# Kernel optimization log

Hardware: AMD Instinct MI355X
Metric: run time of the kernel (lower is better)

## Reference

```python
import jax, jax.numpy as jnp
import numpy as np
import math

MUL = 32
E = 131072
N = 10000
IRREPS = [(0, 1), (1, -1), (2, 1)]  # (l, parity) for 0e + 1o + 2e
SQRT3 = math.sqrt(3.0)

_f = math.factorial


def _w3j_symbol(j1, j2, j3, m1, m2, m3):
    """Standard (complex-basis) Wigner 3j symbol via the Racah formula."""
    if m1 + m2 + m3 != 0:
        return 0.0
    if abs(m1) > j1 or abs(m2) > j2 or abs(m3) > j3:
        return 0.0
    if not (abs(j1 - j2) <= j3 <= j1 + j2):
        return 0.0
    tri = _f(j1 + j2 - j3) * _f(j1 - j2 + j3) * _f(-j1 + j2 + j3) / _f(j1 + j2 + j3 + 1)
    pref = (-1) ** (j1 - j2 - m3) * math.sqrt(
        tri * _f(j1 + m1) * _f(j1 - m1) * _f(j2 + m2) * _f(j2 - m2) * _f(j3 + m3) * _f(j3 - m3)
    )
    tmin = max(0, j2 - j3 - m1, j1 - j3 + m2)
    tmax = min(j1 + j2 - j3, j1 - m1, j2 + m2)
    s = 0.0
    for t in range(tmin, tmax + 1):
        s += (-1) ** t / (
            _f(t) * _f(j3 - j2 + t + m1) * _f(j3 - j1 + t - m2)
            * _f(j1 + j2 - j3 - t) * _f(j1 - t - m1) * _f(j2 - t + m2)
        )
    return pref * s


def _real_basis(l):
    """Complex -> real spherical-harmonic change of basis, rows m=-l..l."""
    U = np.zeros((2 * l + 1, 2 * l + 1), dtype=np.complex128)
    U[l, l] = 1.0
    s = 1.0 / math.sqrt(2.0)
    for m in range(1, l + 1):
        U[l + m, l + m] = ((-1) ** m) * s
        U[l + m, l - m] = s
        U[l - m, l - m] = 1j * s
        U[l - m, l + m] = -1j * ((-1) ** m) * s
    return U


def _w3j_real(l1, l2, l3):
    """Real-basis Wigner 3j tensor, Frobenius norm 1 (e3nn normalization)."""
    Wc = np.zeros((2 * l1 + 1, 2 * l2 + 1, 2 * l3 + 1), dtype=np.complex128)
    for m1 in range(-l1, l1 + 1):
        for m2 in range(-l2, l2 + 1):
            for m3 in range(-l3, l3 + 1):
                Wc[l1 + m1, l2 + m2, l3 + m3] = _w3j_symbol(l1, l2, l3, m1, m2, m3)
    C = np.einsum('im,jn,ko,mno->ijk', _real_basis(l1), _real_basis(l2), _real_basis(l3), Wc)
    re, im = C.real, C.imag
    R = re if np.linalg.norm(re) >= np.linalg.norm(im) else im
    return R / np.linalg.norm(R)


def _build_w3j():
    dims = [2 * l + 1 for l, _ in IRREPS]
    offs = np.concatenate([[0], np.cumsum(dims)])[:-1]
    base_dim = int(sum(dims))  # 9
    # auto-generated instructions: same loop order as the torch module
    ins = []
    for io, (lo, po) in enumerate(IRREPS):
        for i1, (l1, p1) in enumerate(IRREPS):
            for i2, (l2, p2) in enumerate(IRREPS):
                if p1 * p2 == po and abs(l1 - l2) <= lo <= l1 + l2:
                    ins.append((i1, i2, io))
    P = len(ins)  # 11 paths
    w3j = np.zeros((P, base_dim, base_dim, base_dim), dtype=np.float32)
    for p, (i1, i2, io) in enumerate(ins):
        l1, l2, lo = IRREPS[i1][0], IRREPS[i2][0], IRREPS[io][0]
        C = _w3j_real(l1, l2, lo) * math.sqrt(2 * lo + 1)  # component normalization
        w3j[p, offs[i1]:offs[i1] + dims[i1], offs[i2]:offs[i2] + dims[i2], offs[io]:offs[io] + dims[io]] = C
    return w3j


def setup_inputs() -> dict:
    key = jax.random.key(0)
    k1, k2, k3, k4 = jax.random.split(key, 4)
    w3j = jnp.asarray(_build_w3j())  # [P=11, 9, 9, 9]
    P = w3j.shape[0]
    base_dim = w3j.shape[1]
    return {
        'x1': jax.random.normal(k1, (E, MUL * base_dim), dtype=jnp.float32),
        'x2': jax.random.normal(k2, (E, MUL * base_dim), dtype=jnp.float32),
        'idxs': jax.random.randint(k3, (E,), 0, N),
        'weights': jax.random.uniform(k4, (MUL, P), dtype=jnp.float32, minval=-SQRT3, maxval=SQRT3),
        'w3j': w3j,
        'scatter_dim_size': N,
    }


def reference(x1, x2, idxs, weights, w3j, scatter_dim_size):
    base1 = w3j.shape[1]
    base2 = w3j.shape[2]
    # scatter edges -> nodes, then gather back per edge (neighbor sum per center)
    x2s = jax.ops.segment_sum(x2, idxs, num_segments=int(scatter_dim_size))
    x2g = x2s[idxs]
    x1r = x1.reshape(-1, MUL, base1)   # [E, u, i]
    x2r = x2g.reshape(-1, MUL, base2)  # [E, u, j]
    # path-channel coupled weighting: 'up,pijk->uijk'
    ww3j = jnp.einsum('up,pijk->uijk', weights, w3j)
    # out[e,u,k] = sum_ij x1[e,u,i] x2[e,u,j] ww3j[u,i,j,k]
    out = jnp.einsum('eui,euj,uijk->euk', x1r, x2r, ww3j)
    return out
```

## Files before the change

### kernel.cpp

```cpp
#include <hip/hip_runtime.h>

#define MULV 32
#define BASE 9
#define ROW 288
#define NPATH 11
#define W3J_SZ 729
#define PACK_STRIDE 96
#define PACK_TOTAL (MULV * PACK_STRIDE)
#define TILE 64
#define QCOL 72
#define LSTR 73

typedef float f4a4 __attribute__((ext_vector_type(4), aligned(4)));

__device__ constexpr int p_o1[NPATH] = {0,1,4, 0,1,1,4, 0,1,4,4};
__device__ constexpr int p_d1[NPATH] = {1,3,5, 1,3,3,5, 1,3,5,5};
__device__ constexpr int p_o2[NPATH] = {0,1,4, 1,0,4,1, 4,1,0,4};
__device__ constexpr int p_d2[NPATH] = {1,3,5, 3,1,5,3, 5,3,1,5};
__device__ constexpr int p_o3[NPATH] = {0,0,0, 1,1,1,1, 4,4,4,4};
__device__ constexpr int p_d3[NPATH] = {1,1,1, 3,3,3,3, 5,5,5,5};
__device__ constexpr int p_l1[NPATH] = {0,1,2, 0,1,1,2, 0,1,2,2};
__device__ constexpr int p_l2[NPATH] = {0,1,2, 1,0,2,1, 2,1,0,2};
__device__ constexpr int p_l3[NPATH] = {0,0,0, 1,1,1,1, 2,2,2,2};

__device__ __host__ constexpr bool cell_nz(int p, int i, int j, int k) {
    int m1 = i - p_l1[p], m2 = j - p_l2[p], m3 = k - p_l3[p];
    if ((((m1 < 0) + (m2 < 0) + (m3 < 0)) & 1) != 0) return false;
    int a1 = m1 < 0 ? -m1 : m1, a2 = m2 < 0 ? -m2 : m2, a3 = m3 < 0 ? -m3 : m3;
    int d = a1 - a2; if (d < 0) d = -d;
    return (a3 == a1 + a2) || (a3 == d);
}
__device__ __host__ constexpr bool pair_nz(int p, int i, int j) {
    for (int k = 0; k < p_d3[p]; ++k) if (cell_nz(p, i, j, k)) return true;
    return false;
}


__global__ void zero_count_kernel(float* __restrict__ ws, const int* __restrict__ dN) {
    int N = dN[0];
    int* count = (int*)(ws + PACK_TOTAL + (long)N * ROW);
    for (int i = blockIdx.x * blockDim.x + threadIdx.x; i < N; i += gridDim.x * blockDim.x)
        count[i] = 0;
}

__global__ void hist_kernel(const int* __restrict__ idxs, float* __restrict__ ws,
                            const int* __restrict__ dN, int E) {
    int N = dN[0];
    int* count = (int*)(ws + PACK_TOTAL + (long)N * ROW);
    int t = blockIdx.x * blockDim.x + threadIdx.x;
    if (t < E) atomicAdd(&count[idxs[t]], 1);
}

__global__ void scan_kernel(float* __restrict__ ws, const int* __restrict__ dN) {
    int N = dN[0];
    int* count  = (int*)(ws + PACK_TOTAL + (long)N * ROW);
    int* offset = count + N;
    int* cursor = count + 2 * N;
    __shared__ int tsum[256];
    const int tid = threadIdx.x;
    int cpt = (N + 255) / 256;
    int lo = tid * cpt;
    int hi = lo + cpt; if (hi > N) hi = N;
    int s = 0;
    for (int i = lo; i < hi; ++i) s += count[i];
    int v = s;
    tsum[tid] = v;
    __syncthreads();
    #pragma unroll
    for (int off = 1; off < 256; off <<= 1) {
        int t = (tid >= off) ? tsum[tid - off] : 0;
        __syncthreads();
        v += t;
        tsum[tid] = v;
        __syncthreads();
    }
    int run = v - s;
    for (int i = lo; i < hi; ++i) {
        int c = count[i];
        offset[i] = run; cursor[i] = run;
        run += c;
    }
}

__global__ void fill_kernel(const int* __restrict__ idxs, float* __restrict__ ws,
                            const int* __restrict__ dN, int E) {
    int N = dN[0];
    int* count  = (int*)(ws + PACK_TOTAL + (long)N * ROW);
    int* cursor = count + 2 * N;
    int* bucket = count + 3 * N;
    int t = blockIdx.x * blockDim.x + threadIdx.x;
    if (t < E) {
        int n = idxs[t];
        int pos = atomicAdd(&cursor[n], 1);
        bucket[pos] = t;
    }
}

__global__ __launch_bounds__(256) void gather_sum_kernel(const float* __restrict__ x2,
                                                         float* __restrict__ ws,
                                                         const int* __restrict__ dN) {
    int N = dN[0];
    float* x2s  = ws + PACK_TOTAL;
    int* count  = (int*)(x2s + (long)N * ROW);
    int* offset = count + N;
    int* bucket = count + 3 * N;
    const int lane = threadIdx.x & 63;
    const int wv   = threadIdx.x >> 6;
    for (int n0 = blockIdx.x * 4 + wv; n0 < N; n0 += gridDim.x * 4) {
        int n   = __builtin_amdgcn_readfirstlane(n0);
        int off = offset[n];
        int deg = count[n];
        float4 a0 = make_float4(0.f, 0.f, 0.f, 0.f);
        float4 a1 = make_float4(0.f, 0.f, 0.f, 0.f);
        for (int d = 0; d < deg; ++d) {
            int e = bucket[off + d];
            const float4* row = (const float4*)(x2 + (long)e * ROW);
            float4 v = row[lane];
            a0.x += v.x; a0.y += v.y; a0.z += v.z; a0.w += v.w;
            if (lane < 8) {
                float4 w = row[64 + lane];
                a1.x += w.x; a1.y += w.y; a1.z += w.z; a1.w += w.w;
            }
        }
        float4* orow = (float4*)(x2s + (long)n * ROW);
        orow[lane] = a0;
        if (lane < 8) orow[64 + lane] = a1;
    }
}

__global__ void ww_build_kernel(const float* __restrict__ weights,
                                const float* __restrict__ w3j,
                                float* __restrict__ packed) {
    int u = threadIdx.x;
    if (u >= MULV) return;
    int ci = 0;
    #pragma unroll
    for (int p = 0; p < NPATH; ++p) {
        float wgt = weights[u * NPATH + p];
        #pragma unroll
        for (int i = 0; i < p_d1[p]; ++i)
            #pragma unroll
            for (int j = 0; j < p_d2[p]; ++j)
                #pragma unroll
                for (int k = 0; k < p_d3[p]; ++k)
                    if (cell_nz(p, i, j, k)) {
                        int idx = (p_o1[p] + i) * 81 + (p_o2[p] + j) * 9 + (p_o3[p] + k);
                        packed[u * PACK_STRIDE + ci] = wgt * w3j[p * W3J_SZ + idx];
                        ++ci;
                    }
    }
}

__global__ __launch_bounds__(256, 8) void contract_kernel(
    const float* __restrict__ x1, const int* __restrict__ idxs,
    float* __restrict__ ws, const int* __restrict__ dN,
    float* __restrict__ out, int E)
{
    __shared__ float tile[TILE * LSTR];
    __shared__ int lperm[TILE];
    const int tid = threadIdx.x;
    const long ebase = (long)blockIdx.x * TILE;
    const float* __restrict__ packed = ws;
    const float* __restrict__ x2s    = ws + PACK_TOTAL;
    const int N = dN[0];
    const int* __restrict__ bucket = (const int*)(x2s + (long)N * ROW) + 3 * N;

    if (tid < TILE) {
        long ee = ebase + tid;
        lperm[tid] = (ee < (long)E) ? bucket[ee] : -1;
    }
    __syncthreads();

    const int lane = tid & 63;
    const int wv   = __builtin_amdgcn_readfirstlane(tid >> 6);
    const int e    = lperm[lane];
    const bool vld = (e >= 0);
    const int n = idxs[vld ? e : 0];
    const float* __restrict__ r2 = x2s + (long)n * ROW;
    float* __restrict__ lrow = &tile[lane * LSTR];

    float x2c[BASE];
    {
        const float* s = r2 + wv * BASE;
        f4a4 a = *(const f4a4*)s;
        f4a4 b = *(const f4a4*)(s + 4);
        x2c[0]=a.x; x2c[1]=a.y; x2c[2]=a.z; x2c[3]=a.w;
        x2c[4]=b.x; x2c[5]=b.y; x2c[6]=b.z; x2c[7]=b.w;
        x2c[8]=s[8];
    }

    #pragma unroll 1
    for (int h = 0; h < 4; ++h) {
        for (int q = tid; q < TILE * (QCOL / 4); q += 256) {
            int r = q / (QCOL / 4);
            int c = q - r * (QCOL / 4);
            int er = lperm[r];
            if (er >= 0) {
                float4 v = *(const float4*)(x1 + (long)er * ROW + h * QCOL + c * 4);
                float* d = &tile[r * LSTR + c * 4];
                d[0] = v.x; d[1] = v.y; d[2] = v.z; d[3] = v.w;
            }
        }
        __syncthreads();

        #pragma unroll 1
        for (int cc = 0; cc < 2; ++cc) {
            const int u = 8 * h + cc * 4 + wv;
            const float* __restrict__ wp = packed + u * PACK_STRIDE;

            float x2n[BASE];
            if (u + 4 < MULV) {
                const float* s = r2 + (u + 4) * BASE;
                f4a4 a = *(const f4a4*)s;
                f4a4 b = *(const f4a4*)(s + 4);
                x2n[0]=a.x; x2n[1]=a.y; x2n[2]=a.z; x2n[3]=a.w;
                x2n[4]=b.x; x2n[5]=b.y; x2n[6]=b.z; x2n[7]=b.w;
                x2n[8]=s[8];
            }

            const int lbase = (cc * 4 + wv) * BASE;
            float x1v[BASE], acc[BASE];
            #pragma unroll
            for (int i = 0; i < BASE; ++i) {
                x1v[i] = lrow[lbase + i];
                acc[i] = 0.0f;
            }

            int ci = 0;
            #pragma unroll
            for (int p = 0; p < NPATH; ++p) {
                #pragma unroll
                for (int i = 0; i < p_d1[p]; ++i) {
                    #pragma unroll
                    for (int j = 0; j < p_d2[p]; ++j) {
                        if (pair_nz(p, i, j)) {
                            float xx = x1v[p_o1[p] + i] * x2c[p_o2[p] + j];
                            #pragma unroll
                            for (int k = 0; k < p_d3[p]; ++k) {
                                if (cell_nz(p, i, j, k)) {
                                    acc[p_o3[p] + k] = fmaf(wp[ci], xx, acc[p_o3[p] + k]);
                                    ++ci;
                                }
                            }
                        }
                    }
                }
            }
            #pragma unroll
            for (int k = 0; k < BASE; ++k)
                lrow[lbase + k] = acc[k];
            if (u + 4 < MULV) {
                #pragma unroll
                for (int i = 0; i < BASE; ++i) x2c[i] = x2n[i];
            }
        }
        __syncthreads();

        for (int q = tid; q < TILE * (QCOL / 4); q += 256) {
            int r = q / (QCOL / 4);
            int c = q - r * (QCOL / 4);
            int er = lperm[r];
            if (er >= 0) {
                const float* s = &tile[r * LSTR + c * 4];
                *(float4*)(out + (long)er * ROW + h * QCOL + c * 4) =
                    make_float4(s[0], s[1], s[2], s[3]);
            }
        }
        __syncthreads();
    }
}

extern "C" void kernel_launch(void* const* d_in, const int* in_sizes, int n_in,
                              void* d_out, int out_size, void* d_ws, size_t ws_size,
                              hipStream_t stream) {
    const float* x1      = (const float*)d_in[0];
    const float* x2      = (const float*)d_in[1];
    const int*   idxs    = (const int*)d_in[2];
    const float* weights = (const float*)d_in[3];
    const float* w3j     = (const float*)d_in[4];
    const int*   dN      = (const int*)d_in[5];
    float* out = (float*)d_out;
    float* ws  = (float*)d_ws;

    const int E = in_sizes[2];
    const int eb = (E + 255) / 256;

    zero_count_kernel<<<256, 256, 0, stream>>>(ws, dN);
    hist_kernel<<<eb, 256, 0, stream>>>(idxs, ws, dN, E);
    scan_kernel<<<1, 256, 0, stream>>>(ws, dN);
    fill_kernel<<<eb, 256, 0, stream>>>(idxs, ws, dN, E);

    gather_sum_kernel<<<2048, 256, 0, stream>>>(x2, ws, dN);

    ww_build_kernel<<<1, 64, 0, stream>>>(weights, w3j, ws);

    contract_kernel<<<(E + TILE - 1) / TILE, 256, 0, stream>>>(x1, idxs, ws, dN, out, E);
}
```

Before: 196.2 us.

## Prefetch next x1 chunk into registers during contraction and retune launches

The contract kernel now loads the next 72-column x1 chunk into registers while the current chunk is being contracted, rather than loading each chunk only after the previous one finishes. The trailing barrier is dropped because each thread's store and fill use the same tile slots. x2 rows are now loaded per iteration instead of being double-buffered. Launch bounds drop to 4 blocks per SM to make room for the extra registers, at some risk to occupancy. The scan kernel grows to 1024 threads and the gather grid to 2500 blocks.

```diff
diff --git a/kernel.cpp b/kernel.cpp
--- a/kernel.cpp
+++ b/kernel.cpp
@@ -10,6 +10,8 @@
 #define TILE 64
 #define QCOL 72
 #define LSTR 73
+#define NQ4 18
+#define QTOT (TILE * NQ4)
 
 typedef float f4a4 __attribute__((ext_vector_type(4), aligned(4)));
 
@@ -56,9 +58,9 @@
     int* count  = (int*)(ws + PACK_TOTAL + (long)N * ROW);
     int* offset = count + N;
     int* cursor = count + 2 * N;
-    __shared__ int tsum[256];
+    __shared__ int tsum[1024];
     const int tid = threadIdx.x;
-    int cpt = (N + 255) / 256;
+    int cpt = (N + 1023) / 1024;
     int lo = tid * cpt;
     int hi = lo + cpt; if (hi > N) hi = N;
     int s = 0;
@@ -67,7 +69,7 @@
     tsum[tid] = v;
     __syncthreads();
     #pragma unroll
-    for (int off = 1; off < 256; off <<= 1) {
+    for (int off = 1; off < 1024; off <<= 1) {
         int t = (tid >= off) ? tsum[tid - off] : 0;
         __syncthreads();
         v += t;
@@ -151,7 +153,7 @@
     }
 }
 
-__global__ __launch_bounds__(256, 8) void contract_kernel(
+__global__ __launch_bounds__(256, 4) void contract_kernel(
     const float* __restrict__ x1, const int* __restrict__ idxs,
     float* __restrict__ ws, const int* __restrict__ dN,
     float* __restrict__ out, int E)
@@ -174,48 +176,61 @@
     const int lane = tid & 63;
     const int wv   = __builtin_amdgcn_readfirstlane(tid >> 6);
     const int e    = lperm[lane];
-    const bool vld = (e >= 0);
-    const int n = idxs[vld ? e : 0];
+    const int n    = idxs[e >= 0 ? e : 0];
     const float* __restrict__ r2 = x2s + (long)n * ROW;
     float* __restrict__ lrow = &tile[lane * LSTR];
 
-    float x2c[BASE];
-    {
-        const float* s = r2 + wv * BASE;
-        f4a4 a = *(const f4a4*)s;
-        f4a4 b = *(const f4a4*)(s + 4);
-        x2c[0]=a.x; x2c[1]=a.y; x2c[2]=a.z; x2c[3]=a.w;
-        x2c[4]=b.x; x2c[5]=b.y; x2c[6]=b.z; x2c[7]=b.w;
-        x2c[8]=s[8];
+    float4 buf[5];
+    #pragma unroll
+    for (int t = 0; t < 5; ++t) {
+        int q = tid + t * 256;
+        if (q < QTOT) {
+            int r = q / NQ4, c = q - r * NQ4;
+            int er = lperm[r];
+            if (er >= 0)
+                buf[t] = *(const float4*)(x1 + (long)er * ROW + c * 4);
+        }
     }
 
     #pragma unroll 1
     for (int h = 0; h < 4; ++h) {
-        for (int q = tid; q < TILE * (QCOL / 4); q += 256) {
-            int r = q / (QCOL / 4);
-            int c = q - r * (QCOL / 4);
-            int er = lperm[r];
-            if (er >= 0) {
-                float4 v = *(const float4*)(x1 + (long)er * ROW + h * QCOL + c * 4);
+        #pragma unroll
+        for (int t = 0; t < 5; ++t) {
+            int q = tid + t * 256;
+            if (q < QTOT) {
+                int r = q / NQ4, c = q - r * NQ4;
                 float* d = &tile[r * LSTR + c * 4];
-                d[0] = v.x; d[1] = v.y; d[2] = v.z; d[3] = v.w;
+                d[0] = buf[t].x; d[1] = buf[t].y; d[2] = buf[t].z; d[3] = buf[t].w;
             }
         }
         __syncthreads();
+
+        if (h < 3) {
+            #pragma unroll
+            for (int t = 0; t < 5; ++t) {
+                int q = tid + t * 256;
+                if (q < QTOT) {
+                    int r = q / NQ4, c = q - r * NQ4;
+                    int er = lperm[r];
+                    if (er >= 0)
+                        buf[t] = *(const float4*)(x1 + (long)er * ROW + (h + 1) * QCOL + c * 4);
+                }
+            }
+        }
 
         #pragma unroll 1
         for (int cc = 0; cc < 2; ++cc) {
             const int u = 8 * h + cc * 4 + wv;
             const float* __restrict__ wp = packed + u * PACK_STRIDE;
 
-            float x2n[BASE];
-            if (u + 4 < MULV) {
-                const float* s = r2 + (u + 4) * BASE;
+            float x2c[BASE];
+            {
+                const float* s = r2 + u * BASE;
                 f4a4 a = *(const f4a4*)s;
                 f4a4 b = *(const f4a4*)(s + 4);
-                x2n[0]=a.x; x2n[1]=a.y; x2n[2]=a.z; x2n[3]=a.w;
-                x2n[4]=b.x; x2n[5]=b.y; x2n[6]=b.z; x2n[7]=b.w;
-                x2n[8]=s[8];
+                x2c[0]=a.x; x2c[1]=a.y; x2c[2]=a.z; x2c[3]=a.w;
+                x2c[4]=b.x; x2c[5]=b.y; x2c[6]=b.z; x2c[7]=b.w;
+                x2c[8]=s[8];
             }
 
             const int lbase = (cc * 4 + wv) * BASE;
@@ -249,24 +264,22 @@
             #pragma unroll
             for (int k = 0; k < BASE; ++k)
                 lrow[lbase + k] = acc[k];
-            if (u + 4 < MULV) {
-                #pragma unroll
-                for (int i = 0; i < BASE; ++i) x2c[i] = x2n[i];
-            }
         }
         __syncthreads();
 
-        for (int q = tid; q < TILE * (QCOL / 4); q += 256) {
-            int r = q / (QCOL / 4);
-            int c = q - r * (QCOL / 4);
-            int er = lperm[r];
-            if (er >= 0) {
-                const float* s = &tile[r * LSTR + c * 4];
-                *(float4*)(out + (long)er * ROW + h * QCOL + c * 4) =
-                    make_float4(s[0], s[1], s[2], s[3]);
-            }
-        }
-        __syncthreads();
+        #pragma unroll
+        for (int t = 0; t < 5; ++t) {
+            int q = tid + t * 256;
+            if (q < QTOT) {
+                int r = q / NQ4, c = q - r * NQ4;
+                int er = lperm[r];
+                if (er >= 0) {
+                    const float* s = &tile[r * LSTR + c * 4];
+                    *(float4*)(out + (long)er * ROW + h * QCOL + c * 4) =
+                        make_float4(s[0], s[1], s[2], s[3]);
+                }
+            }
+        }
     }
 }
 
@@ -287,10 +300,10 @@
 
     zero_count_kernel<<<256, 256, 0, stream>>>(ws, dN);
     hist_kernel<<<eb, 256, 0, stream>>>(idxs, ws, dN, E);
-    scan_kernel<<<1, 256, 0, stream>>>(ws, dN);
+    scan_kernel<<<1, 1024, 0, stream>>>(ws, dN);
     fill_kernel<<<eb, 256, 0, stream>>>(idxs, ws, dN, E);
 
-    gather_sum_kernel<<<2048, 256, 0, stream>>>(x2, ws, dN);
+    gather_sum_kernel<<<2500, 256, 0, stream>>>(x2, ws, dN);
 
     ww_build_kernel<<<1, 64, 0, stream>>>(weights, w3j, ws);
 
```

New measurement: 179.9 us. 8.3% less time.
